# Performance work log

Measured on AMD Instinct MI355X. Metric: run time of the kernel, lower is better.

Reference implementation:

```python
import jax, jax.numpy as jnp
import numpy as np

B_, L_, D_MODEL = 2, 4096, 1024
D_STATE, D_CONV, D_INNER = 64, 4, 2048
EPS = 1.1920929e-07  # torch.finfo(float32).eps, nn.RMSNorm default


def setup_inputs() -> dict:
    key = jax.random.key(0)
    ks = jax.random.split(key, 8)
    s = 0.02
    x = jax.random.normal(ks[0], (B_, L_, D_MODEL), jnp.float32)
    W_in = jax.random.normal(ks[1], (D_MODEL, 2 * D_INNER), jnp.float32) * s
    conv_w = jax.random.normal(ks[2], (D_INNER, 1, D_CONV), jnp.float32) * s  # depthwise (O,I/g,K)
    conv_b = jnp.zeros((D_INNER,), jnp.float32)
    W_x = jax.random.normal(ks[3], (D_INNER, 2 * D_STATE + D_INNER), jnp.float32) * s
    W_dt = jax.random.normal(ks[4], (D_INNER, D_INNER), jnp.float32) * s
    b_dt = jnp.zeros((D_INNER,), jnp.float32)
    A_log = jnp.log(jnp.tile(jnp.arange(1, D_STATE + 1, dtype=jnp.float32)[None, :], (D_INNER, 1)))
    D_param = jnp.ones((D_INNER,), jnp.float32)
    W_out = jax.random.normal(ks[5], (D_INNER, D_MODEL), jnp.float32) * s
    norm_w = jnp.ones((D_INNER,), jnp.float32)
    return dict(x=x, W_in=W_in, conv_w=conv_w, conv_b=conv_b, W_x=W_x, W_dt=W_dt,
                b_dt=b_dt, A_log=A_log, D_param=D_param, W_out=W_out, norm_w=norm_w)


def selective_scan(x_conv, dt, A, B_ssm, C_ssm, D_param):
    # x_conv,dt: (B,L,d_inner); A:(d_inner,d_state); B_ssm,C_ssm:(B,L,d_state)
    dt = jax.nn.softplus(dt)

    def step(h, inp):
        dt_t, B_t, C_t, x_t = inp  # (B,di),(B,ds),(B,ds),(B,di)
        dA = jnp.exp(dt_t[:, :, None] * A[None, :, :])           # (B,di,ds)
        h = dA * h + (dt_t * x_t)[:, :, None] * B_t[:, None, :]  # (B,di,ds)
        y = jnp.einsum('bds,bs->bd', h, C_t)                     # (B,di)
        return h, y

    h0 = jnp.zeros((x_conv.shape[0], A.shape[0], A.shape[1]), x_conv.dtype)
    xs = (jnp.moveaxis(dt, 1, 0), jnp.moveaxis(B_ssm, 1, 0),
          jnp.moveaxis(C_ssm, 1, 0), jnp.moveaxis(x_conv, 1, 0))
    _, ys = jax.lax.scan(step, h0, xs)
    y = jnp.moveaxis(ys, 0, 1)  # (B,L,d_inner)
    return y + x_conv * D_param[None, None, :]


def reference(x, W_in, conv_w, conv_b, W_x, W_dt, b_dt, A_log, D_param, W_out, norm_w):
    xz = x @ W_in                                    # (B,L,2*d_inner)
    x_ssm, z = jnp.split(xz, 2, axis=-1)
    # causal depthwise conv1d: left-pad d_conv-1 == torch pad-both-then-slice[:L]
    xc = jnp.swapaxes(x_ssm, 1, 2)                   # (B,d_inner,L)
    xc = jax.lax.conv_general_dilated(
        xc, conv_w, window_strides=(1,), padding=[(D_CONV - 1, 0)],
        dimension_numbers=('NCH', 'OIH', 'NCH'), feature_group_count=D_INNER)
    xc = xc + conv_b[None, :, None]
    xc = jax.nn.silu(jnp.swapaxes(xc, 1, 2))         # (B,L,d_inner)
    dbc = xc @ W_x                                   # (B,L,2*d_state+d_inner)
    B_ssm = dbc[..., :D_STATE]
    C_ssm = dbc[..., D_STATE:2 * D_STATE]
    dt = dbc[..., 2 * D_STATE:] @ W_dt + b_dt
    A = -jnp.exp(A_log)
    y = selective_scan(xc, dt, A, B_ssm, C_ssm, D_param)
    # RMSNorm then gate
    y = y * jax.lax.rsqrt(jnp.mean(y * y, axis=-1, keepdims=True) + EPS) * norm_w
    y = y * jax.nn.silu(z)
    return y @ W_out
```

## Files before the change

### kernel.cpp

```cpp
#include <hip/hip_runtime.h>
#include <hip/hip_bf16.h>

#define L_SEQ   4096
#define DMODEL  1024
#define DINNER  2048
#define DSTATE  64
#define NB      2
#define DPB     128
#define DBCS    2304
#define NROWS   (NB * L_SEQ)

typedef unsigned short u16;
typedef __attribute__((ext_vector_type(8))) short bf16x8;
typedef __attribute__((ext_vector_type(4))) float f32x4;
typedef __attribute__((ext_vector_type(2))) float f32x2;

__device__ __forceinline__ float silu_f(float x)  { return x / (1.f + __expf(-x)); }
__device__ __forceinline__ float softplus_f(float x) {
    return x > 15.f ? x : __logf(1.f + __expf(x));
}
__device__ __forceinline__ float bf2f(u16 u) { return __uint_as_float(((unsigned)u) << 16); }
__device__ __forceinline__ u16 f2bf(float f) {
    __hip_bfloat16 h = __float2bfloat16(f);
    return *reinterpret_cast<u16*>(&h);
}
__device__ __forceinline__ unsigned pack2(float a, float b) {
    return (unsigned)f2bf(a) | ((unsigned)f2bf(b) << 16);
}

__global__ __launch_bounds__(256) void f32_to_bf16_kernel(
    const float* __restrict__ in, u16* __restrict__ out)
{
    const int i = (blockIdx.x * 256 + threadIdx.x) * 4;
    float4 v = *reinterpret_cast<const float4*>(in + i);
    ushort4 o;
    o.x = f2bf(v.x); o.y = f2bf(v.y); o.z = f2bf(v.z); o.w = f2bf(v.w);
    *reinterpret_cast<ushort4*>(out + i) = o;
}

__global__ __launch_bounds__(256) void transpose_bf16_kernel(
    const float* __restrict__ W, u16* __restrict__ Wt, int K, int N)
{
    __shared__ float t[32][33];
    const int n0 = blockIdx.x * 32, k0 = blockIdx.y * 32;
    const int tx = threadIdx.x & 31, ty = threadIdx.x >> 5;
    #pragma unroll
    for (int i = 0; i < 32; i += 8)
        t[ty + i][tx] = W[(size_t)(k0 + ty + i) * N + n0 + tx];
    __syncthreads();
    #pragma unroll
    for (int i = 0; i < 32; i += 8)
        Wt[(size_t)(n0 + ty + i) * K + k0 + tx] = f2bf(t[tx][ty + i]);
}

__global__ __launch_bounds__(256) void bias_cat_kernel(
    const float* __restrict__ b_dt, float* __restrict__ bias)
{
    const int i = blockIdx.x * 256 + threadIdx.x;
    float v = 0.f;
    if (i >= 128 && i < 128 + DINNER) v = b_dt[i - 128];
    bias[i] = v;
}

template <typename TC>
__global__ __launch_bounds__(256) void mfma_gemm(
    const u16* __restrict__ A, int lda,
    const u16* __restrict__ Bt, int ldb,
    TC* __restrict__ C, int ldc,
    int K, const float* __restrict__ bias)
{
    __shared__ u16 As[128 * 32];
    __shared__ u16 Bs[128 * 32];
    const int tid  = threadIdx.x;
    const int lane = tid & 63;
    const int w    = tid >> 6;
    const int wm   = w >> 1, wn = w & 1;

    const int gx = gridDim.x;
    const int nwg = gx * gridDim.y;
    int wg = blockIdx.y * gx + blockIdx.x;
    if ((nwg & 7) == 0) wg = (wg & 7) * (nwg >> 3) + (wg >> 3);
    const int bm = (wg / gx) * 128, bn = (wg % gx) * 128;

    const int lr = lane & 15, lk = lane >> 4;
    const int srow  = lane >> 2;
    const int scolb = (lane & 3) * 16;
    const size_t ldaB = (size_t)lda * 2, ldbB = (size_t)ldb * 2;

    const char* Ab = (const char*)A + (size_t)bm * ldaB;
    const char* Bb = (const char*)Bt + (size_t)bn * ldbB;
    char* AsB = (char*)As;
    char* BsB = (char*)Bs;

    f32x4 acc[4][4] = {};

    for (int k0 = 0; k0 < K; k0 += 32) {
        const size_t kb = (size_t)k0 * 2;
        #pragma unroll
        for (int i = 0; i < 2; ++i) {
            const int row = i * 64 + w * 16 + srow;
            __builtin_amdgcn_global_load_lds(
                (const __attribute__((address_space(1))) void*)(Ab + (size_t)row * ldaB + kb + scolb),
                (__attribute__((address_space(3))) void*)(AsB + i * 4096 + w * 1024),
                16, 0, 0);
            __builtin_amdgcn_global_load_lds(
                (const __attribute__((address_space(1))) void*)(Bb + (size_t)row * ldbB + kb + scolb),
                (__attribute__((address_space(3))) void*)(BsB + i * 4096 + w * 1024),
                16, 0, 0);
        }
        __syncthreads();
        bf16x8 a[4], b[4];
        #pragma unroll
        for (int mi = 0; mi < 4; ++mi)
            a[mi] = *reinterpret_cast<const bf16x8*>(&As[(wm * 64 + mi * 16 + lr) * 32 + lk * 8]);
        #pragma unroll
        for (int ni = 0; ni < 4; ++ni)
            b[ni] = *reinterpret_cast<const bf16x8*>(&Bs[(wn * 64 + ni * 16 + lr) * 32 + lk * 8]);
        #pragma unroll
        for (int mi = 0; mi < 4; ++mi)
            #pragma unroll
            for (int ni = 0; ni < 4; ++ni)
                acc[mi][ni] = __builtin_amdgcn_mfma_f32_16x16x32_bf16(a[mi], b[ni], acc[mi][ni], 0, 0, 0);
        __syncthreads();
    }

    float bv[4];
    if (bias) {
        #pragma unroll
        for (int ni = 0; ni < 4; ++ni) bv[ni] = bias[bn + wn * 64 + ni * 16 + lr];
    }
    #pragma unroll
    for (int mi = 0; mi < 4; ++mi) {
        #pragma unroll
        for (int ni = 0; ni < 4; ++ni) {
            #pragma unroll
            for (int r = 0; r < 4; ++r) {
                const int row = bm + wm * 64 + mi * 16 + lk * 4 + r;
                const int col = bn + wn * 64 + ni * 16 + lr;
                float v = acc[mi][ni][r];
                if (bias) v += bv[ni];
                if constexpr (sizeof(TC) == 4) C[(size_t)row * ldc + col] = v;
                else                           C[(size_t)row * ldc + col] = f2bf(v);
            }
        }
    }
}

#define BAR()  asm volatile("s_barrier" ::: "memory")
#define WV(n)  asm volatile("s_waitcnt vmcnt(" #n ")" ::: "memory")
#define STG16(s, d) __builtin_amdgcn_global_load_lds( \
    (const __attribute__((address_space(1))) void*)(s), \
    (__attribute__((address_space(3))) void*)(d), 16, 0, 0)

template <typename TC, int ACT>
__global__ __launch_bounds__(512, 2) void gemm256(
    const u16* __restrict__ A, int lda,
    const u16* __restrict__ Bt, int ldb,
    TC* __restrict__ C, int ldc,
    int K, const float* __restrict__ bias)
{
    extern __shared__ char lds[];
    const int tid = threadIdx.x;
    const int l = tid & 63, w = tid >> 6;
    const int wm = w >> 2, wn = w & 3;
    const int lr = l & 15, lk = l >> 4;

    const int gx = gridDim.x;
    const int nwg = gx * gridDim.y;
    int wg = blockIdx.y * gx + blockIdx.x;
    wg = (wg & 7) * (nwg >> 3) + (wg >> 3);
    const int bm = (wg / gx) * 256, bn = (wg % gx) * 256;

    const size_t ldaB = (size_t)lda * 2, ldbB = (size_t)ldb * 2;
    const int gsw = (((l & 7) ^ (l >> 3)) << 4);
    const char* aSrc = (const char*)A + (size_t)(bm + w * 8 + (l >> 3)) * ldaB + gsw;
    const char* bSrc = (const char*)Bt + (size_t)(bn + w * 8 + (l >> 3)) * ldbB + gsw;
    const int csw0 = (lk * 16) ^ ((lr & 7) << 4);
    const int wdst = w * 1024;

    const int nk = K >> 6;
    f32x4 acc[8][4] = {};

    {
        STG16(aSrc + (size_t)(0 * 64) * ldaB, lds + 0 * 8192 + wdst);
        STG16(aSrc + (size_t)(2 * 64) * ldaB, lds + 2 * 8192 + wdst);
        STG16(bSrc + (size_t)(0 * 64) * ldbB, lds + 32768 + 0 * 8192 + wdst);
        STG16(bSrc + (size_t)(1 * 64) * ldbB, lds + 32768 + 1 * 8192 + wdst);
        STG16(bSrc + (size_t)(2 * 64) * ldbB, lds + 32768 + 2 * 8192 + wdst);
        STG16(bSrc + (size_t)(3 * 64) * ldbB, lds + 32768 + 3 * 8192 + wdst);
        STG16(aSrc + (size_t)(1 * 64) * ldaB, lds + 1 * 8192 + wdst);
        STG16(aSrc + (size_t)(3 * 64) * ldaB, lds + 3 * 8192 + wdst);
        WV(2);
        BAR();
    }

    for (int t = 0; t < nk; ++t) {
        const int p = t & 1;
        const char* Ar = lds + (p << 16);
        const char* Br = Ar + 32768;
        const int tn = (t + 1 < nk) ? t + 1 : t;
        char* dq = lds + (((t + 1) & 1) << 16);
        const size_t Tb = (size_t)tn << 7;
        const char* aS = aSrc + Tb;
        const char* bS = bSrc + Tb;

        bf16x8 a[4][2], bf[2][2];

        #pragma unroll
        for (int mi = 0; mi < 4; ++mi) {
            const int ro = (wm * 128 + mi * 16 + lr) * 128;
            a[mi][0] = *reinterpret_cast<const bf16x8*>(Ar + ro + csw0);
            a[mi][1] = *reinterpret_cast<const bf16x8*>(Ar + ro + (csw0 ^ 64));
        }
        #pragma unroll
        for (int ni = 0; ni < 2; ++ni) {
            const int ro = (wn * 64 + ni * 16 + lr) * 128;
            bf[ni][0] = *reinterpret_cast<const bf16x8*>(Br + ro + csw0);
            bf[ni][1] = *reinterpret_cast<const bf16x8*>(Br + ro + (csw0 ^ 64));
        }
        STG16(aS + (size_t)(0 * 64) * ldaB, dq + 0 * 8192 + wdst);
        STG16(aS + (size_t)(2 * 64) * ldaB, dq + 2 * 8192 + wdst);
        BAR();
        __builtin_amdgcn_s_setprio(1);
        #pragma unroll
        for (int mi = 0; mi < 4; ++mi)
            #pragma unroll
            for (int ni = 0; ni < 2; ++ni) {
                acc[mi][ni] = __builtin_amdgcn_mfma_f32_16x16x32_bf16(a[mi][0], bf[ni][0], acc[mi][ni], 0, 0, 0);
                acc[mi][ni] = __builtin_amdgcn_mfma_f32_16x16x32_bf16(a[mi][1], bf[ni][1], acc[mi][ni], 0, 0, 0);
            }
        __builtin_amdgcn_s_setprio(0);
        BAR();

        #pragma unroll
        for (int ni = 0; ni < 2; ++ni) {
            const int ro = (wn * 64 + (2 + ni) * 16 + lr) * 128;
            bf[ni][0] = *reinterpret_cast<const bf16x8*>(Br + ro + csw0);
            bf[ni][1] = *reinterpret_cast<const bf16x8*>(Br + ro + (csw0 ^ 64));
        }
        STG16(bS + (size_t)(0 * 64) * ldbB, dq + 32768 + 0 * 8192 + wdst);
        STG16(bS + (size_t)(1 * 64) * ldbB, dq + 32768 + 1 * 8192 + wdst);
        BAR();
        __builtin_amdgcn_s_setprio(1);
        #pragma unroll
        for (int mi = 0; mi < 4; ++mi)
            #pragma unroll
            for (int ni = 0; ni < 2; ++ni) {
                acc[mi][2 + ni] = __builtin_amdgcn_mfma_f32_16x16x32_bf16(a[mi][0], bf[ni][0], acc[mi][2 + ni], 0, 0, 0);
                acc[mi][2 + ni] = __builtin_amdgcn_mfma_f32_16x16x32_bf16(a[mi][1], bf[ni][1], acc[mi][2 + ni], 0, 0, 0);
            }
        __builtin_amdgcn_s_setprio(0);
        WV(4);
        BAR();

        #pragma unroll
        for (int mi = 0; mi < 4; ++mi) {
            const int ro = (wm * 128 + (4 + mi) * 16 + lr) * 128;
            a[mi][0] = *reinterpret_cast<const bf16x8*>(Ar + ro + csw0);
            a[mi][1] = *reinterpret_cast<const bf16x8*>(Ar + ro + (csw0 ^ 64));
        }
        STG16(bS + (size_t)(2 * 64) * ldbB, dq + 32768 + 2 * 8192 + wdst);
        STG16(bS + (size_t)(3 * 64) * ldbB, dq + 32768 + 3 * 8192 + wdst);
        BAR();
        __builtin_amdgcn_s_setprio(1);
        #pragma unroll
        for (int mi = 0; mi < 4; ++mi)
            #pragma unroll
            for (int ni = 0; ni < 2; ++ni) {
                acc[4 + mi][2 + ni] = __builtin_amdgcn_mfma_f32_16x16x32_bf16(a[mi][0], bf[ni][0], acc[4 + mi][2 + ni], 0, 0, 0);
                acc[4 + mi][2 + ni] = __builtin_amdgcn_mfma_f32_16x16x32_bf16(a[mi][1], bf[ni][1], acc[4 + mi][2 + ni], 0, 0, 0);
            }
        __builtin_amdgcn_s_setprio(0);
        BAR();

        #pragma unroll
        for (int ni = 0; ni < 2; ++ni) {
            const int ro = (wn * 64 + ni * 16 + lr) * 128;
            bf[ni][0] = *reinterpret_cast<const bf16x8*>(Br + ro + csw0);
            bf[ni][1] = *reinterpret_cast<const bf16x8*>(Br + ro + (csw0 ^ 64));
        }
        STG16(aS + (size_t)(1 * 64) * ldaB, dq + 1 * 8192 + wdst);
        STG16(aS + (size_t)(3 * 64) * ldaB, dq + 3 * 8192 + wdst);
        BAR();
        __builtin_amdgcn_s_setprio(1);
        #pragma unroll
        for (int mi = 0; mi < 4; ++mi)
            #pragma unroll
            for (int ni = 0; ni < 2; ++ni) {
                acc[4 + mi][ni] = __builtin_amdgcn_mfma_f32_16x16x32_bf16(a[mi][0], bf[ni][0], acc[4 + mi][ni], 0, 0, 0);
                acc[4 + mi][ni] = __builtin_amdgcn_mfma_f32_16x16x32_bf16(a[mi][1], bf[ni][1], acc[4 + mi][ni], 0, 0, 0);
            }
        __builtin_amdgcn_s_setprio(0);
        WV(2);
        BAR();
    }

    float bv[4];
    if (bias) {
        #pragma unroll
        for (int ni = 0; ni < 4; ++ni) bv[ni] = bias[bn + wn * 64 + ni * 16 + lr];
    }
    #pragma unroll
    for (int mi = 0; mi < 8; ++mi) {
        #pragma unroll
        for (int ni = 0; ni < 4; ++ni) {
            #pragma unroll
            for (int r = 0; r < 4; ++r) {
                const int row = bm + wm * 128 + mi * 16 + lk * 4 + r;
                const int col = bn + wn * 64 + ni * 16 + lr;
                float v = acc[mi][ni][r];
                if (bias) v += bv[ni];
                if constexpr (ACT == 2) { if (col >= 128) v = softplus_f(v); }
                if constexpr (sizeof(TC) == 4) C[(size_t)row * ldc + col] = v;
                else                           C[(size_t)row * ldc + col] = f2bf(v);
            }
        }
    }
}

__global__ __launch_bounds__(256) void conv_silu_kernel(
    const u16* __restrict__ xz, const float* __restrict__ cw,
    const float* __restrict__ cb, u16* __restrict__ xc)
{
    const int idx8 = blockIdx.x * 256 + threadIdx.x;
    const int db  = (idx8 & 255) << 3;
    const int row = idx8 >> 8;
    const int l   = row & (L_SEQ - 1);

    float v[4][8];
    #pragma unroll
    for (int k = 0; k < 4; ++k) {
        const int ll = l - 3 + k;
        if (ll >= 0) {
            uint4 u = *reinterpret_cast<const uint4*>(xz + (size_t)(row - 3 + k) * 4096 + db);
            v[k][0]=bf2f((u16)(u.x&0xffff)); v[k][1]=bf2f((u16)(u.x>>16));
            v[k][2]=bf2f((u16)(u.y&0xffff)); v[k][3]=bf2f((u16)(u.y>>16));
            v[k][4]=bf2f((u16)(u.z&0xffff)); v[k][5]=bf2f((u16)(u.z>>16));
            v[k][6]=bf2f((u16)(u.w&0xffff)); v[k][7]=bf2f((u16)(u.w>>16));
        } else {
            #pragma unroll
            for (int j = 0; j < 8; ++j) v[k][j] = 0.f;
        }
    }
    float acc[8];
    {
        float4 c0 = *reinterpret_cast<const float4*>(cb + db);
        float4 c1 = *reinterpret_cast<const float4*>(cb + db + 4);
        acc[0]=c0.x; acc[1]=c0.y; acc[2]=c0.z; acc[3]=c0.w;
        acc[4]=c1.x; acc[5]=c1.y; acc[6]=c1.z; acc[7]=c1.w;
    }
    #pragma unroll
    for (int j = 0; j < 8; ++j) {
        const float4 wv = reinterpret_cast<const float4*>(cw)[db + j];
        acc[j] = fmaf(v[0][j], wv.x, acc[j]);
        acc[j] = fmaf(v[1][j], wv.y, acc[j]);
        acc[j] = fmaf(v[2][j], wv.z, acc[j]);
        acc[j] = fmaf(v[3][j], wv.w, acc[j]);
    }
    uint4 o;
    o.x = pack2(silu_f(acc[0]), silu_f(acc[1]));
    o.y = pack2(silu_f(acc[2]), silu_f(acc[3]));
    o.z = pack2(silu_f(acc[4]), silu_f(acc[5]));
    o.w = pack2(silu_f(acc[6]), silu_f(acc[7]));
    *reinterpret_cast<uint4*>(xc + (size_t)row * 2048 + db) = o;
}


__device__ __forceinline__ int a_pattern_check_half(
    const float* A_log, int d, int base, float& A0)
{
    A0 = -__expf(A_log[d * DSTATE]);
    int ok = 1;
    #pragma unroll
    for (int j = 0; j < 32; ++j) {
        const int s = base + j;
        const float As = -__expf(A_log[d * DSTATE + s]);
        ok &= (fabsf(As - A0 * (float)(s + 1)) <= 1e-3f * (float)(s + 1));
    }
    return ok;
}

#define UNPACK8(dstp, u)  do {                                             \
    float4 _a, _b;                                                         \
    _a.x=bf2f((u16)((u).x&0xffff)); _a.y=bf2f((u16)((u).x>>16));           \
    _a.z=bf2f((u16)((u).y&0xffff)); _a.w=bf2f((u16)((u).y>>16));           \
    _b.x=bf2f((u16)((u).z&0xffff)); _b.y=bf2f((u16)((u).z>>16));           \
    _b.z=bf2f((u16)((u).w&0xffff)); _b.w=bf2f((u16)((u).w>>16));           \
    *reinterpret_cast<float4*>(dstp) = _a;                                 \
    *reinterpret_cast<float4*>((dstp) + 4) = _b;                           \
} while (0)

__global__ __launch_bounds__(256) void scan_phase1(
    const u16* __restrict__ xc,
    const u16* __restrict__ dbc,
    const float* __restrict__ A_log,
    float* __restrict__ hend, float* __restrict__ sumdt,
    int nchunk, int chunk)
{
    const int tid  = threadIdx.x;
    const int dl   = tid >> 1, half = tid & 1;
    const int base = half * 32;
    const int d0   = blockIdx.x * DPB;
    const int d    = d0 + dl;
    const int c = blockIdx.y, b = blockIdx.z;
    const int t0 = c * chunk;
    const size_t bL = (size_t)b * L_SEQ;

    __shared__ float dts_s[16][132];
    __shared__ float xcs_s[16][132];
    __shared__ float Bs_s[16][68];

    float A0;
    int fast = a_pattern_check_half(A_log, d, base, A0);
    fast = __syncthreads_and(fast);

    f32x2 h2[16];
    #pragma unroll
    for (int j = 0; j < 16; ++j) h2[j] = (f32x2){0.f, 0.f};
    float sd = 0.f;

    for (int ts = 0; ts < chunk; ts += 16) {
        __syncthreads();
        {
            const int rr = tid >> 4, cc = (tid & 15) * 8;
            const size_t row = bL + t0 + ts + rr;
            uint4 v = *reinterpret_cast<const uint4*>(dbc + row * DBCS + 128 + d0 + cc);
            UNPACK8(&dts_s[rr][cc], v);
            uint4 u = *reinterpret_cast<const uint4*>(xc + row * 2048 + d0 + cc);
            UNPACK8(&xcs_s[rr][cc], u);
        }
        if (tid < 128) {
            const int rr = tid >> 3, cc = (tid & 7) * 8;
            const size_t row = bL + t0 + ts + rr;
            uint4 v = *reinterpret_cast<const uint4*>(dbc + row * DBCS + cc);
            UNPACK8(&Bs_s[rr][cc], v);
        }
        __syncthreads();
        if (fast) {
            for (int r = 0; r < 16; ++r) {
                const float dts = dts_s[r][dl];
                const float xv  = xcs_s[r][dl];
                const float dtx = dts * xv;
                sd += dts;
                const float q  = __expf(A0 * dts);
                const float q2 = q * q, q3 = q2 * q, q4 = q2 * q2;
                const float q8 = q4 * q4, q16 = q8 * q8, q32 = q16 * q16;
                const float qb = half ? q32 : 1.f;
                f32x2 pA = {qb * q, qb * q2};
                f32x2 pB = {qb * q3, qb * q4};
                const f32x2 q44 = {q4, q4};
                const f32x2 dtx2 = {dtx, dtx};
                #pragma unroll
                for (int g = 0; g < 8; ++g) {
                    const f32x2 B01 = *reinterpret_cast<const f32x2*>(&Bs_s[r][base + g * 4]);
                    const f32x2 B23 = *reinterpret_cast<const f32x2*>(&Bs_s[r][base + g * 4 + 2]);
                    h2[2*g]   = pA * h2[2*g]   + B01 * dtx2;
                    h2[2*g+1] = pB * h2[2*g+1] + B23 * dtx2;
                    pA = pA * q44; pB = pB * q44;
                }
            }
        } else {
            float* hs = (float*)h2;
            for (int r = 0; r < 16; ++r) {
                const float dts = dts_s[r][dl];
                const float xv  = xcs_s[r][dl];
                const float dtx = dts * xv;
                sd += dts;
                #pragma unroll
                for (int j = 0; j < 32; ++j) {
                    const float a = __expf(-__expf(A_log[d * DSTATE + base + j]) * dts);
                    hs[j] = fmaf(a, hs[j], dtx * Bs_s[r][base + j]);
                }
            }
        }
    }
    const size_t cb64 = ((size_t)b * nchunk + c) * DSTATE;
    const float* hs = (const float*)h2;
    #pragma unroll
    for (int j = 0; j < 32; ++j) hend[(cb64 + base + j) * DINNER + d] = hs[j];
    if (half == 0) sumdt[((size_t)b * nchunk + c) * DINNER + d] = sd;
}

__global__ __launch_bounds__(256) void scan_phase2(
    float* __restrict__ hbuf, const float* __restrict__ sumdt,
    const float* __restrict__ A_log, int nchunk)
{
    const int idx = blockIdx.x * 256 + threadIdx.x;
    const int d = idx & (DINNER - 1);
    const int s = (idx >> 11) & (DSTATE - 1);
    const int b = idx >> 17;

    const float A = -__expf(A_log[d * DSTATE + s]);
    float h = 0.f;
    for (int c = 0; c < nchunk; ++c) {
        const size_t off = (((size_t)b * nchunk + c) * DSTATE + s) * DINNER + d;
        const float he = hbuf[off];
        const float ap = __expf(A * sumdt[((size_t)b * nchunk + c) * DINNER + d]);
        hbuf[off] = h;
        h = fmaf(ap, h, he);
    }
}

__global__ __launch_bounds__(256) void scan_phase3(
    u16* __restrict__ xc,
    const u16* __restrict__ dbc,
    const float* __restrict__ A_log,
    const float* __restrict__ hinit,
    const float* __restrict__ D_param,
    int nchunk, int chunk)
{
    const int tid  = threadIdx.x;
    const int dl   = tid >> 1, half = tid & 1;
    const int base = half * 32;
    const int d0   = blockIdx.x * DPB;
    const int d    = d0 + dl;
    const int c = blockIdx.y, b = blockIdx.z;
    const int t0 = c * chunk;
    const size_t bL = (size_t)b * L_SEQ;

    __shared__ float dts_s[16][132];
    __shared__ float xcs_s[16][132];
    __shared__ float BCs[16][132];

    float A0;
    int fast = a_pattern_check_half(A_log, d, base, A0);
    fast = __syncthreads_and(fast);

    f32x2 h2[16];
    {
        const size_t cb64 = ((size_t)b * nchunk + c) * DSTATE;
        float* hs = (float*)h2;
        #pragma unroll
        for (int j = 0; j < 32; ++j) hs[j] = hinit[(cb64 + base + j) * DINNER + d];
    }
    const float Dp = D_param[d];

    for (int ts = 0; ts < chunk; ts += 16) {
        __syncthreads();
        {
            const int rr = tid >> 4, cc = (tid & 15) * 8;
            const size_t row = bL + t0 + ts + rr;
            uint4 v = *reinterpret_cast<const uint4*>(dbc + row * DBCS + 128 + d0 + cc);
            UNPACK8(&dts_s[rr][cc], v);
            uint4 u = *reinterpret_cast<const uint4*>(xc + row * 2048 + d0 + cc);
            UNPACK8(&xcs_s[rr][cc], u);
            uint4 w = *reinterpret_cast<const uint4*>(dbc + row * DBCS + cc);
            UNPACK8(&BCs[rr][cc], w);
        }
        __syncthreads();
        if (fast) {
            for (int r = 0; r < 16; ++r) {
                const float dts = dts_s[r][dl];
                const float xv  = xcs_s[r][dl];
                const float dtx = dts * xv;
                const float q  = __expf(A0 * dts);
                const float q2 = q * q, q3 = q2 * q, q4 = q2 * q2;
                const float q8 = q4 * q4, q16 = q8 * q8, q32 = q16 * q16;
                const float qb = half ? q32 : 1.f;
                f32x2 pA = {qb * q, qb * q2};
                f32x2 pB = {qb * q3, qb * q4};
                const f32x2 q44 = {q4, q4};
                const f32x2 dtx2 = {dtx, dtx};
                f32x2 y2 = {0.f, 0.f};
                #pragma unroll
                for (int g = 0; g < 8; ++g) {
                    const f32x2 B01 = *reinterpret_cast<const f32x2*>(&BCs[r][base + g * 4]);
                    const f32x2 B23 = *reinterpret_cast<const f32x2*>(&BCs[r][base + g * 4 + 2]);
                    const f32x2 C01 = *reinterpret_cast<const f32x2*>(&BCs[r][64 + base + g * 4]);
                    const f32x2 C23 = *reinterpret_cast<const f32x2*>(&BCs[r][64 + base + g * 4 + 2]);
                    h2[2*g]   = pA * h2[2*g]   + B01 * dtx2;
                    h2[2*g+1] = pB * h2[2*g+1] + B23 * dtx2;
                    y2 = h2[2*g] * C01 + y2;
                    y2 = h2[2*g+1] * C23 + y2;
                    pA = pA * q44; pB = pB * q44;
                }
                float y = y2.x + y2.y;
                const float yt = y + __shfl_xor(y, 1, 64);
                if (half == 0) {
                    const size_t row = bL + t0 + ts + r;
                    xc[row * 2048 + d] = f2bf(fmaf(xv, Dp, yt));
                }
            }
        } else {
            float* hs = (float*)h2;
            for (int r = 0; r < 16; ++r) {
                const float dts = dts_s[r][dl];
                const float xv  = xcs_s[r][dl];
                const float dtx = dts * xv;
                float y = 0.f;
                #pragma unroll
                for (int j = 0; j < 32; ++j) {
                    const float a = __expf(-__expf(A_log[d * DSTATE + base + j]) * dts);
                    hs[j] = fmaf(a, hs[j], dtx * BCs[r][base + j]);
                    y = fmaf(hs[j], BCs[r][64 + base + j], y);
                }
                const float yt = y + __shfl_xor(y, 1, 64);
                if (half == 0) {
                    const size_t row = bL + t0 + ts + r;
                    xc[row * 2048 + d] = f2bf(fmaf(xv, Dp, yt));
                }
            }
        }
    }
}

__global__ __launch_bounds__(256) void rms_gate_kernel(
    u16* __restrict__ y, const u16* __restrict__ xz,
    const float* __restrict__ norm_w)
{
    const int row = blockIdx.x;
    const int tid = threadIdx.x;
    const size_t ybase = (size_t)row * DINNER;
    const size_t zbase = (size_t)row * 4096 + DINNER;
    const int i8 = tid * 8;

    float yv[8];
    {
        uint4 u = *reinterpret_cast<const uint4*>(y + ybase + i8);
        yv[0]=bf2f((u16)(u.x&0xffff)); yv[1]=bf2f((u16)(u.x>>16));
        yv[2]=bf2f((u16)(u.y&0xffff)); yv[3]=bf2f((u16)(u.y>>16));
        yv[4]=bf2f((u16)(u.z&0xffff)); yv[5]=bf2f((u16)(u.z>>16));
        yv[6]=bf2f((u16)(u.w&0xffff)); yv[7]=bf2f((u16)(u.w>>16));
    }
    float ss = 0.f;
    #pragma unroll
    for (int j = 0; j < 8; ++j) ss = fmaf(yv[j], yv[j], ss);
    #pragma unroll
    for (int off = 32; off > 0; off >>= 1) ss += __shfl_down(ss, off, 64);
    __shared__ float sred[4];
    const int lane = tid & 63, wid = tid >> 6;
    if (lane == 0) sred[wid] = ss;
    __syncthreads();
    const float tot = sred[0] + sred[1] + sred[2] + sred[3];
    const float scale = rsqrtf(tot * (1.f / (float)DINNER) + 1.1920929e-07f);

    float zv[8];
    {
        uint4 u = *reinterpret_cast<const uint4*>(xz + zbase + i8);
        zv[0]=bf2f((u16)(u.x&0xffff)); zv[1]=bf2f((u16)(u.x>>16));
        zv[2]=bf2f((u16)(u.y&0xffff)); zv[3]=bf2f((u16)(u.y>>16));
        zv[4]=bf2f((u16)(u.z&0xffff)); zv[5]=bf2f((u16)(u.z>>16));
        zv[6]=bf2f((u16)(u.w&0xffff)); zv[7]=bf2f((u16)(u.w>>16));
    }
    float4 n0 = *reinterpret_cast<const float4*>(norm_w + i8);
    float4 n1 = *reinterpret_cast<const float4*>(norm_w + i8 + 4);
    const float nw[8] = {n0.x,n0.y,n0.z,n0.w,n1.x,n1.y,n1.z,n1.w};
    float o[8];
    #pragma unroll
    for (int j = 0; j < 8; ++j) o[j] = yv[j] * scale * nw[j] * silu_f(zv[j]);
    uint4 ov;
    ov.x = pack2(o[0], o[1]); ov.y = pack2(o[2], o[3]);
    ov.z = pack2(o[4], o[5]); ov.w = pack2(o[6], o[7]);
    *reinterpret_cast<uint4*>(y + ybase + i8) = ov;
}

extern "C" void kernel_launch(void* const* d_in, const int* in_sizes, int n_in,
                              void* d_out, int out_size, void* d_ws, size_t ws_size,
                              hipStream_t stream)
{
    const float* x       = (const float*)d_in[0];
    const float* W_in    = (const float*)d_in[1];
    const float* conv_w  = (const float*)d_in[2];
    const float* conv_b  = (const float*)d_in[3];
    const float* W_x     = (const float*)d_in[4];
    const float* W_dt    = (const float*)d_in[5];
    const float* b_dt    = (const float*)d_in[6];
    const float* A_log   = (const float*)d_in[7];
    const float* D_param = (const float*)d_in[8];
    const float* W_out   = (const float*)d_in[9];
    const float* norm_w  = (const float*)d_in[10];
    float* out = (float*)d_out;

    hipFuncSetAttribute(reinterpret_cast<const void*>(&gemm256<u16, 0>),
                        hipFuncAttributeMaxDynamicSharedMemorySize, 131072);
    hipFuncSetAttribute(reinterpret_cast<const void*>(&gemm256<u16, 2>),
                        hipFuncAttributeMaxDynamicSharedMemorySize, 131072);

    char* ws = (char*)d_ws;
    u16* xz  = (u16*)(ws);
    u16* xc  = (u16*)(ws + 67108864ull);
    u16* dbc = (u16*)(ws + 100663296ull);
    u16* xbf  = dbc;
    u16* Wxbf = xz;
    u16* Wt_out = (u16*)(ws + 138412032ull);
    float* bias2304 = (float*)(ws + 142606336ull);
    const size_t fixed_bytes = 142615552ull;
    const size_t per_chunk = 2ull * DSTATE * DINNER * 4 + 2ull * DINNER * 4;
    int nchunk = 64;
    while (nchunk > 1 && fixed_bytes + (size_t)nchunk * per_chunk > ws_size) nchunk >>= 1;
    const int chunk = L_SEQ / nchunk;
    float* hbuf = (float*)(ws + fixed_bytes);
    float* sdt  = (float*)(ws + fixed_bytes + (size_t)nchunk * 2ull * DSTATE * DINNER * 4);

    u16* Wt_in = (u16*)d_out;
    u16* Wt_x  = Wt_in + 4194304ull;
    u16* Wt_dt = Wt_x + 4718592ull;

    const int M = NROWS;

    f32_to_bf16_kernel<<<(M * DMODEL) / 1024, 256, 0, stream>>>(x, xbf);
    f32_to_bf16_kernel<<<(DINNER * 2176) / 1024, 256, 0, stream>>>(W_x, Wxbf);
    transpose_bf16_kernel<<<dim3(4096 / 32, 1024 / 32), 256, 0, stream>>>(W_in, Wt_in, 1024, 4096);
    transpose_bf16_kernel<<<dim3(4, 2048 / 32), 256, 0, stream>>>(W_x, Wt_x, 2048, 2176);
    transpose_bf16_kernel<<<dim3(2048 / 32, 2048 / 32), 256, 0, stream>>>(W_dt, Wt_dt, 2048, 2048);
    transpose_bf16_kernel<<<dim3(1024 / 32, 2048 / 32), 256, 0, stream>>>(W_out, Wt_out, 2048, 1024);
    bias_cat_kernel<<<9, 256, 0, stream>>>(b_dt, bias2304);
    hipMemsetAsync(Wt_x + 2176ull * 2048, 0, 128ull * 2048 * 2, stream);
    mfma_gemm<u16><<<dim3(2048 / 128, 2048 / 128), 256, 0, stream>>>(
        Wt_dt, 2048, Wxbf + 128, 2176, Wt_x + 128ull * 2048, 2048, 2048, nullptr);

    gemm256<u16, 0><<<dim3(4096 / 256, M / 256), 512, 131072, stream>>>(
        xbf, DMODEL, Wt_in, DMODEL, xz, 4096, DMODEL, nullptr);
    conv_silu_kernel<<<(M * DINNER) / (256 * 8), 256, 0, stream>>>(xz, conv_w, conv_b, xc);
    gemm256<u16, 2><<<dim3(DBCS / 256, M / 256), 512, 131072, stream>>>(
        xc, DINNER, Wt_x, DINNER, dbc, DBCS, DINNER, bias2304);
    scan_phase1<<<dim3(DINNER / DPB, nchunk, NB), 256, 0, stream>>>(
        xc, dbc, A_log, hbuf, sdt, nchunk, chunk);
    scan_phase2<<<(NB * DINNER * DSTATE) / 256, 256, 0, stream>>>(hbuf, sdt, A_log, nchunk);
    scan_phase3<<<dim3(DINNER / DPB, nchunk, NB), 256, 0, stream>>>(
        xc, dbc, A_log, hbuf, D_param, nchunk, chunk);
    rms_gate_kernel<<<M, 256, 0, stream>>>(xc, xz, norm_w);
    mfma_gemm<float><<<dim3(1024 / 128, M / 128), 256, 0, stream>>>(
        xc, DINNER, Wt_out, DINNER, out, DMODEL, DINNER, nullptr);
}
```

Before: 654.0 us.

## Use 256-tile GEMM for weight fusion and output projection, widen scan LDS reads

Replaces the 128x128 mfma_gemm with the pipelined 256x256 gemm256 kernel for the W_dt·W_x weight-fusion GEMM and for the final output projection, then deletes the old kernel. The scan kernels now read B/C from shared memory as 4-wide vectors instead of pairs of 2-wide loads. The scan chunk count drops from 64 to 32. The larger GEMM tiles give fewer workgroups for the output projection (128 WGs of 512 threads), which may underfill the GPU. Halving the chunk count lengthens the sequential scan per chunk and shrinks the phase-2 carry work.

```diff
diff --git a/kernel.cpp b/kernel.cpp
--- a/kernel.cpp
+++ b/kernel.cpp
@@ -60,90 +60,6 @@
     float v = 0.f;
     if (i >= 128 && i < 128 + DINNER) v = b_dt[i - 128];
     bias[i] = v;
-}
-
-template <typename TC>
-__global__ __launch_bounds__(256) void mfma_gemm(
-    const u16* __restrict__ A, int lda,
-    const u16* __restrict__ Bt, int ldb,
-    TC* __restrict__ C, int ldc,
-    int K, const float* __restrict__ bias)
-{
-    __shared__ u16 As[128 * 32];
-    __shared__ u16 Bs[128 * 32];
-    const int tid  = threadIdx.x;
-    const int lane = tid & 63;
-    const int w    = tid >> 6;
-    const int wm   = w >> 1, wn = w & 1;
-
-    const int gx = gridDim.x;
-    const int nwg = gx * gridDim.y;
-    int wg = blockIdx.y * gx + blockIdx.x;
-    if ((nwg & 7) == 0) wg = (wg & 7) * (nwg >> 3) + (wg >> 3);
-    const int bm = (wg / gx) * 128, bn = (wg % gx) * 128;
-
-    const int lr = lane & 15, lk = lane >> 4;
-    const int srow  = lane >> 2;
-    const int scolb = (lane & 3) * 16;
-    const size_t ldaB = (size_t)lda * 2, ldbB = (size_t)ldb * 2;
-
-    const char* Ab = (const char*)A + (size_t)bm * ldaB;
-    const char* Bb = (const char*)Bt + (size_t)bn * ldbB;
-    char* AsB = (char*)As;
-    char* BsB = (char*)Bs;
-
-    f32x4 acc[4][4] = {};
-
-    for (int k0 = 0; k0 < K; k0 += 32) {
-        const size_t kb = (size_t)k0 * 2;
-        #pragma unroll
-        for (int i = 0; i < 2; ++i) {
-            const int row = i * 64 + w * 16 + srow;
-            __builtin_amdgcn_global_load_lds(
-                (const __attribute__((address_space(1))) void*)(Ab + (size_t)row * ldaB + kb + scolb),
-                (__attribute__((address_space(3))) void*)(AsB + i * 4096 + w * 1024),
-                16, 0, 0);
-            __builtin_amdgcn_global_load_lds(
-                (const __attribute__((address_space(1))) void*)(Bb + (size_t)row * ldbB + kb + scolb),
-                (__attribute__((address_space(3))) void*)(BsB + i * 4096 + w * 1024),
-                16, 0, 0);
-        }
-        __syncthreads();
-        bf16x8 a[4], b[4];
-        #pragma unroll
-        for (int mi = 0; mi < 4; ++mi)
-            a[mi] = *reinterpret_cast<const bf16x8*>(&As[(wm * 64 + mi * 16 + lr) * 32 + lk * 8]);
-        #pragma unroll
-        for (int ni = 0; ni < 4; ++ni)
-            b[ni] = *reinterpret_cast<const bf16x8*>(&Bs[(wn * 64 + ni * 16 + lr) * 32 + lk * 8]);
-        #pragma unroll
-        for (int mi = 0; mi < 4; ++mi)
-            #pragma unroll
-            for (int ni = 0; ni < 4; ++ni)
-                acc[mi][ni] = __builtin_amdgcn_mfma_f32_16x16x32_bf16(a[mi], b[ni], acc[mi][ni], 0, 0, 0);
-        __syncthreads();
-    }
-
-    float bv[4];
-    if (bias) {
-        #pragma unroll
-        for (int ni = 0; ni < 4; ++ni) bv[ni] = bias[bn + wn * 64 + ni * 16 + lr];
-    }
-    #pragma unroll
-    for (int mi = 0; mi < 4; ++mi) {
-        #pragma unroll
-        for (int ni = 0; ni < 4; ++ni) {
-            #pragma unroll
-            for (int r = 0; r < 4; ++r) {
-                const int row = bm + wm * 64 + mi * 16 + lk * 4 + r;
-                const int col = bn + wn * 64 + ni * 16 + lr;
-                float v = acc[mi][ni][r];
-                if (bias) v += bv[ni];
-                if constexpr (sizeof(TC) == 4) C[(size_t)row * ldc + col] = v;
-                else                           C[(size_t)row * ldc + col] = f2bf(v);
-            }
-        }
-    }
 }
 
 #define BAR()  asm volatile("s_barrier" ::: "memory")
@@ -430,10 +346,10 @@
             UNPACK8(&xcs_s[rr][cc], u);
         }
         if (tid < 128) {
-            const int rr = tid >> 3, cc = (tid & 7) * 8;
-            const size_t row = bL + t0 + ts + rr;
-            uint4 v = *reinterpret_cast<const uint4*>(dbc + row * DBCS + cc);
-            UNPACK8(&Bs_s[rr][cc], v);
+            const int rb = tid >> 3, cb = (tid & 7) * 8;
+            const size_t row = bL + t0 + ts + rb;
+            uint4 v = *reinterpret_cast<const uint4*>(dbc + row * DBCS + cb);
+            UNPACK8(&Bs_s[rb][cb], v);
         }
         __syncthreads();
         if (fast) {
@@ -452,8 +368,9 @@
                 const f32x2 dtx2 = {dtx, dtx};
                 #pragma unroll
                 for (int g = 0; g < 8; ++g) {
-                    const f32x2 B01 = *reinterpret_cast<const f32x2*>(&Bs_s[r][base + g * 4]);
-                    const f32x2 B23 = *reinterpret_cast<const f32x2*>(&Bs_s[r][base + g * 4 + 2]);
+                    const f32x4 Bq = *reinterpret_cast<const f32x4*>(&Bs_s[r][base + g * 4]);
+                    const f32x2 B01 = {Bq[0], Bq[1]};
+                    const f32x2 B23 = {Bq[2], Bq[3]};
                     h2[2*g]   = pA * h2[2*g]   + B01 * dtx2;
                     h2[2*g+1] = pB * h2[2*g+1] + B23 * dtx2;
                     pA = pA * q44; pB = pB * q44;
@@ -564,10 +481,12 @@
                 f32x2 y2 = {0.f, 0.f};
                 #pragma unroll
                 for (int g = 0; g < 8; ++g) {
-                    const f32x2 B01 = *reinterpret_cast<const f32x2*>(&BCs[r][base + g * 4]);
-                    const f32x2 B23 = *reinterpret_cast<const f32x2*>(&BCs[r][base + g * 4 + 2]);
-                    const f32x2 C01 = *reinterpret_cast<const f32x2*>(&BCs[r][64 + base + g * 4]);
-                    const f32x2 C23 = *reinterpret_cast<const f32x2*>(&BCs[r][64 + base + g * 4 + 2]);
+                    const f32x4 Bq = *reinterpret_cast<const f32x4*>(&BCs[r][base + g * 4]);
+                    const f32x4 Cq = *reinterpret_cast<const f32x4*>(&BCs[r][64 + base + g * 4]);
+                    const f32x2 B01 = {Bq[0], Bq[1]};
+                    const f32x2 B23 = {Bq[2], Bq[3]};
+                    const f32x2 C01 = {Cq[0], Cq[1]};
+                    const f32x2 C23 = {Cq[2], Cq[3]};
                     h2[2*g]   = pA * h2[2*g]   + B01 * dtx2;
                     h2[2*g+1] = pB * h2[2*g+1] + B23 * dtx2;
                     y2 = h2[2*g] * C01 + y2;
@@ -675,6 +594,8 @@
                         hipFuncAttributeMaxDynamicSharedMemorySize, 131072);
     hipFuncSetAttribute(reinterpret_cast<const void*>(&gemm256<u16, 2>),
                         hipFuncAttributeMaxDynamicSharedMemorySize, 131072);
+    hipFuncSetAttribute(reinterpret_cast<const void*>(&gemm256<float, 0>),
+                        hipFuncAttributeMaxDynamicSharedMemorySize, 131072);
 
     char* ws = (char*)d_ws;
     u16* xz  = (u16*)(ws);
@@ -686,7 +607,7 @@
     float* bias2304 = (float*)(ws + 142606336ull);
     const size_t fixed_bytes = 142615552ull;
     const size_t per_chunk = 2ull * DSTATE * DINNER * 4 + 2ull * DINNER * 4;
-    int nchunk = 64;
+    int nchunk = 32;
     while (nchunk > 1 && fixed_bytes + (size_t)nchunk * per_chunk > ws_size) nchunk >>= 1;
     const int chunk = L_SEQ / nchunk;
     float* hbuf = (float*)(ws + fixed_bytes);
@@ -706,7 +627,7 @@
     transpose_bf16_kernel<<<dim3(1024 / 32, 2048 / 32), 256, 0, stream>>>(W_out, Wt_out, 2048, 1024);
     bias_cat_kernel<<<9, 256, 0, stream>>>(b_dt, bias2304);
     hipMemsetAsync(Wt_x + 2176ull * 2048, 0, 128ull * 2048 * 2, stream);
-    mfma_gemm<u16><<<dim3(2048 / 128, 2048 / 128), 256, 0, stream>>>(
+    gemm256<u16, 0><<<dim3(2048 / 256, 2048 / 256), 512, 131072, stream>>>(
         Wt_dt, 2048, Wxbf + 128, 2176, Wt_x + 128ull * 2048, 2048, 2048, nullptr);
 
     gemm256<u16, 0><<<dim3(4096 / 256, M / 256), 512, 131072, stream>>>(
@@ -720,6 +641,6 @@
     scan_phase3<<<dim3(DINNER / DPB, nchunk, NB), 256, 0, stream>>>(
         xc, dbc, A_log, hbuf, D_param, nchunk, chunk);
     rms_gate_kernel<<<M, 256, 0, stream>>>(xc, xz, norm_w);
-    mfma_gemm<float><<<dim3(1024 / 128, M / 128), 256, 0, stream>>>(
+    gemm256<float, 0><<<dim3(1024 / 256, M / 256), 512, 131072, stream>>>(
         xc, DINNER, Wt_out, DINNER, out, DMODEL, DINNER, nullptr);
 }
```

New measurement: 644.8 us. About the same (-1.4%).

## Precompute A pattern check, halve scan chunks, use gemm256 for output projection

Applied to the files above, without the earlier changes.

Adds a small kernel that computes A0 and the geometric-pattern flag once per channel, so the scan phases no longer redo 32 exps per thread. The shared-memory B/C reads are widened to 128-bit loads. The chunk count is reduced from 64 to 32, which lowers phase-2 work and hbuf traffic but halves the parallelism available to phases 1 and 3. The final output GEMM switches from the 128-tile mfma_gemm to the larger 256-tile gemm256 kernel, leaving only 128 workgroups for that GEMM.

```diff
diff --git a/kernel.cpp b/kernel.cpp
--- a/kernel.cpp
+++ b/kernel.cpp
@@ -60,6 +60,21 @@
     float v = 0.f;
     if (i >= 128 && i < 128 + DINNER) v = b_dt[i - 128];
     bias[i] = v;
+}
+
+__global__ __launch_bounds__(256) void a0_kernel(
+    const float* __restrict__ A_log, float* __restrict__ A0f,
+    unsigned char* __restrict__ okf)
+{
+    const int d = blockIdx.x * 256 + threadIdx.x;
+    const float A0 = -__expf(A_log[d * DSTATE]);
+    int ok = 1;
+    for (int s = 1; s < DSTATE; ++s) {
+        const float As = -__expf(A_log[d * DSTATE + s]);
+        ok &= (fabsf(As - A0 * (float)(s + 1)) <= 1e-3f * (float)(s + 1));
+    }
+    A0f[d] = A0;
+    okf[d] = (unsigned char)ok;
 }
 
 template <typename TC>
@@ -366,20 +381,6 @@
 }
 
 
-__device__ __forceinline__ int a_pattern_check_half(
-    const float* A_log, int d, int base, float& A0)
-{
-    A0 = -__expf(A_log[d * DSTATE]);
-    int ok = 1;
-    #pragma unroll
-    for (int j = 0; j < 32; ++j) {
-        const int s = base + j;
-        const float As = -__expf(A_log[d * DSTATE + s]);
-        ok &= (fabsf(As - A0 * (float)(s + 1)) <= 1e-3f * (float)(s + 1));
-    }
-    return ok;
-}
-
 #define UNPACK8(dstp, u)  do {                                             \
     float4 _a, _b;                                                         \
     _a.x=bf2f((u16)((u).x&0xffff)); _a.y=bf2f((u16)((u).x>>16));           \
@@ -394,6 +395,7 @@
     const u16* __restrict__ xc,
     const u16* __restrict__ dbc,
     const float* __restrict__ A_log,
+    const float* __restrict__ A0f, const unsigned char* __restrict__ okf,
     float* __restrict__ hend, float* __restrict__ sumdt,
     int nchunk, int chunk)
 {
@@ -410,9 +412,8 @@
     __shared__ float xcs_s[16][132];
     __shared__ float Bs_s[16][68];
 
-    float A0;
-    int fast = a_pattern_check_half(A_log, d, base, A0);
-    fast = __syncthreads_and(fast);
+    const float A0 = A0f[d];
+    int fast = __syncthreads_and((int)okf[d]);
 
     f32x2 h2[16];
     #pragma unroll
@@ -430,10 +431,10 @@
             UNPACK8(&xcs_s[rr][cc], u);
         }
         if (tid < 128) {
-            const int rr = tid >> 3, cc = (tid & 7) * 8;
-            const size_t row = bL + t0 + ts + rr;
-            uint4 v = *reinterpret_cast<const uint4*>(dbc + row * DBCS + cc);
-            UNPACK8(&Bs_s[rr][cc], v);
+            const int rb = tid >> 3, cb = (tid & 7) * 8;
+            const size_t row = bL + t0 + ts + rb;
+            uint4 v = *reinterpret_cast<const uint4*>(dbc + row * DBCS + cb);
+            UNPACK8(&Bs_s[rb][cb], v);
         }
         __syncthreads();
         if (fast) {
@@ -452,8 +453,9 @@
                 const f32x2 dtx2 = {dtx, dtx};
                 #pragma unroll
                 for (int g = 0; g < 8; ++g) {
-                    const f32x2 B01 = *reinterpret_cast<const f32x2*>(&Bs_s[r][base + g * 4]);
-                    const f32x2 B23 = *reinterpret_cast<const f32x2*>(&Bs_s[r][base + g * 4 + 2]);
+                    const f32x4 Bq = *reinterpret_cast<const f32x4*>(&Bs_s[r][base + g * 4]);
+                    const f32x2 B01 = {Bq[0], Bq[1]};
+                    const f32x2 B23 = {Bq[2], Bq[3]};
                     h2[2*g]   = pA * h2[2*g]   + B01 * dtx2;
                     h2[2*g+1] = pB * h2[2*g+1] + B23 * dtx2;
                     pA = pA * q44; pB = pB * q44;
@@ -505,6 +507,7 @@
     u16* __restrict__ xc,
     const u16* __restrict__ dbc,
     const float* __restrict__ A_log,
+    const float* __restrict__ A0f, const unsigned char* __restrict__ okf,
     const float* __restrict__ hinit,
     const float* __restrict__ D_param,
     int nchunk, int chunk)
@@ -522,9 +525,8 @@
     __shared__ float xcs_s[16][132];
     __shared__ float BCs[16][132];
 
-    float A0;
-    int fast = a_pattern_check_half(A_log, d, base, A0);
-    fast = __syncthreads_and(fast);
+    const float A0 = A0f[d];
+    int fast = __syncthreads_and((int)okf[d]);
 
     f32x2 h2[16];
     {
@@ -564,10 +566,12 @@
                 f32x2 y2 = {0.f, 0.f};
                 #pragma unroll
                 for (int g = 0; g < 8; ++g) {
-                    const f32x2 B01 = *reinterpret_cast<const f32x2*>(&BCs[r][base + g * 4]);
-                    const f32x2 B23 = *reinterpret_cast<const f32x2*>(&BCs[r][base + g * 4 + 2]);
-                    const f32x2 C01 = *reinterpret_cast<const f32x2*>(&BCs[r][64 + base + g * 4]);
-                    const f32x2 C23 = *reinterpret_cast<const f32x2*>(&BCs[r][64 + base + g * 4 + 2]);
+                    const f32x4 Bq = *reinterpret_cast<const f32x4*>(&BCs[r][base + g * 4]);
+                    const f32x4 Cq = *reinterpret_cast<const f32x4*>(&BCs[r][64 + base + g * 4]);
+                    const f32x2 B01 = {Bq[0], Bq[1]};
+                    const f32x2 B23 = {Bq[2], Bq[3]};
+                    const f32x2 C01 = {Cq[0], Cq[1]};
+                    const f32x2 C23 = {Cq[2], Cq[3]};
                     h2[2*g]   = pA * h2[2*g]   + B01 * dtx2;
                     h2[2*g+1] = pB * h2[2*g+1] + B23 * dtx2;
                     y2 = h2[2*g] * C01 + y2;
@@ -675,6 +679,8 @@
                         hipFuncAttributeMaxDynamicSharedMemorySize, 131072);
     hipFuncSetAttribute(reinterpret_cast<const void*>(&gemm256<u16, 2>),
                         hipFuncAttributeMaxDynamicSharedMemorySize, 131072);
+    hipFuncSetAttribute(reinterpret_cast<const void*>(&gemm256<float, 0>),
+                        hipFuncAttributeMaxDynamicSharedMemorySize, 131072);
 
     char* ws = (char*)d_ws;
     u16* xz  = (u16*)(ws);
@@ -684,9 +690,11 @@
     u16* Wxbf = xz;
     u16* Wt_out = (u16*)(ws + 138412032ull);
     float* bias2304 = (float*)(ws + 142606336ull);
-    const size_t fixed_bytes = 142615552ull;
+    float* A0f = (float*)(ws + 142615552ull);
+    unsigned char* okf = (unsigned char*)(ws + 142623744ull);
+    const size_t fixed_bytes = 142625792ull;
     const size_t per_chunk = 2ull * DSTATE * DINNER * 4 + 2ull * DINNER * 4;
-    int nchunk = 64;
+    int nchunk = 32;
     while (nchunk > 1 && fixed_bytes + (size_t)nchunk * per_chunk > ws_size) nchunk >>= 1;
     const int chunk = L_SEQ / nchunk;
     float* hbuf = (float*)(ws + fixed_bytes);
@@ -705,6 +713,7 @@
     transpose_bf16_kernel<<<dim3(2048 / 32, 2048 / 32), 256, 0, stream>>>(W_dt, Wt_dt, 2048, 2048);
     transpose_bf16_kernel<<<dim3(1024 / 32, 2048 / 32), 256, 0, stream>>>(W_out, Wt_out, 2048, 1024);
     bias_cat_kernel<<<9, 256, 0, stream>>>(b_dt, bias2304);
+    a0_kernel<<<DINNER / 256, 256, 0, stream>>>(A_log, A0f, okf);
     hipMemsetAsync(Wt_x + 2176ull * 2048, 0, 128ull * 2048 * 2, stream);
     mfma_gemm<u16><<<dim3(2048 / 128, 2048 / 128), 256, 0, stream>>>(
         Wt_dt, 2048, Wxbf + 128, 2176, Wt_x + 128ull * 2048, 2048, 2048, nullptr);
@@ -715,11 +724,11 @@
     gemm256<u16, 2><<<dim3(DBCS / 256, M / 256), 512, 131072, stream>>>(
         xc, DINNER, Wt_x, DINNER, dbc, DBCS, DINNER, bias2304);
     scan_phase1<<<dim3(DINNER / DPB, nchunk, NB), 256, 0, stream>>>(
-        xc, dbc, A_log, hbuf, sdt, nchunk, chunk);
+        xc, dbc, A_log, A0f, okf, hbuf, sdt, nchunk, chunk);
     scan_phase2<<<(NB * DINNER * DSTATE) / 256, 256, 0, stream>>>(hbuf, sdt, A_log, nchunk);
     scan_phase3<<<dim3(DINNER / DPB, nchunk, NB), 256, 0, stream>>>(
-        xc, dbc, A_log, hbuf, D_param, nchunk, chunk);
+        xc, dbc, A_log, A0f, okf, hbuf, D_param, nchunk, chunk);
     rms_gate_kernel<<<M, 256, 0, stream>>>(xc, xz, norm_w);
-    mfma_gemm<float><<<dim3(1024 / 128, M / 128), 256, 0, stream>>>(
+    gemm256<float, 0><<<dim3(1024 / 256, M / 256), 512, 131072, stream>>>(
         xc, DINNER, Wt_out, DINNER, out, DMODEL, DINNER, nullptr);
 }
```

Measured after the change: 629.0 us, median of 2. 1.04x faster.
